# Kernel optimization log

Hardware: AMD Instinct MI355X
Metric: run time of the kernel (lower is better)

## Reference

```python
import jax, jax.numpy as jnp
import numpy as np

NEG_SLOPE = 0.2  # PyG GATConv default leaky_relu slope
EPS = 1e-16      # PyG softmax denominator epsilon


def gat_conv(x, src, dst, n_nodes, W, att_src, att_dst, bias, concat):
    # x: [N, Din]; W: [Din, H*F]; att_src/att_dst: [H, F]; bias: [H*F] or [F]
    H, F = att_src.shape
    h = (x @ W).reshape(n_nodes, H, F)                 # [N, H, F]
    a_src = jnp.einsum('nhf,hf->nh', h, att_src)       # [N, H]
    a_dst = jnp.einsum('nhf,hf->nh', h, att_dst)       # [N, H]
    e = jax.nn.leaky_relu(a_src[src] + a_dst[dst], NEG_SLOPE)  # [E, H]
    # segment softmax over incoming edges of each destination node
    m = jax.ops.segment_max(e, dst, num_segments=n_nodes)      # [N, H]
    ex = jnp.exp(e - m[dst])                                   # [E, H]
    s = jax.ops.segment_sum(ex, dst, num_segments=n_nodes)     # [N, H]
    alpha = ex / (s[dst] + EPS)                                # [E, H]
    msg = alpha[:, :, None] * h[src]                           # [E, H, F]
    out = jax.ops.segment_sum(msg, dst, num_segments=n_nodes)  # [N, H, F]
    if concat:
        out = out.reshape(n_nodes, H * F)
    else:
        out = out.mean(axis=1)
    return out + bias


def setup_inputs() -> dict:
    key = jax.random.key(0)
    ks = jax.random.split(key, 12)
    N, E, Din, Fh, H, C = 50000, 800000, 512, 32, 8, 40
    x = jax.random.normal(ks[0], (N, Din), dtype=jnp.float32)
    edge_index = jax.random.randint(ks[1], (2, E), 0, N, dtype=jnp.int64)
    g1 = 1.0 / np.sqrt(Din)
    g2 = 1.0 / np.sqrt(H * Fh)
    return {
        'x': x,
        'edge_index': edge_index,
        'W1': jax.random.normal(ks[2], (Din, H * Fh), dtype=jnp.float32) * g1,
        'att_src1': jax.random.normal(ks[3], (H, Fh), dtype=jnp.float32) * g2,
        'att_dst1': jax.random.normal(ks[4], (H, Fh), dtype=jnp.float32) * g2,
        'b1': jnp.zeros((H * Fh,), dtype=jnp.float32),
        'W2': jax.random.normal(ks[5], (H * Fh, C), dtype=jnp.float32) * g2,
        'att_src2': jax.random.normal(ks[6], (1, C), dtype=jnp.float32) * 0.1,
        'att_dst2': jax.random.normal(ks[7], (1, C), dtype=jnp.float32) * 0.1,
        'b2': jnp.zeros((C,), dtype=jnp.float32),
    }


def reference(x, edge_index, W1, att_src1, att_dst1, b1, W2, att_src2, att_dst2, b2):
    N = x.shape[0]
    # PyG GATConv adds self-loops by default
    loop = jnp.arange(N, dtype=edge_index.dtype)
    src = jnp.concatenate([edge_index[0], loop])
    dst = jnp.concatenate([edge_index[1], loop])
    # eval mode: dropout layers are identity
    h = gat_conv(x, src, dst, N, W1, att_src1, att_dst1, b1, concat=True)
    h = jax.nn.elu(h)
    out = gat_conv(h, src, dst, N, W2, att_src2, att_dst2, b2, concat=False)
    return jax.nn.log_softmax(out, axis=1)
```

## Files before the change

### kernel.cpp

```cpp
#include <hip/hip_runtime.h>
#include <hip/hip_bf16.h>
#include <math.h>

#define NN_DIN 512
#define NN_HF  256
#define NN_H   8
#define NN_F   32
#define NN_C   40

typedef short bf16x8 __attribute__((ext_vector_type(8)));
typedef float f32x4 __attribute__((ext_vector_type(4)));

__device__ __forceinline__ unsigned short f2bf_rne(float x) {
    unsigned u = __builtin_bit_cast(unsigned, x);
    unsigned r = u + 0x7FFFu + ((u >> 16) & 1u);
    return (unsigned short)(r >> 16);
}
__device__ __forceinline__ float bfu2f(unsigned short s) {
    unsigned u = ((unsigned)s) << 16;
    return __builtin_bit_cast(float, u);
}

__global__ __launch_bounds__(256) void w1rne_kernel(
    const float* __restrict__ W1, unsigned short* __restrict__ Wh)
{
    __shared__ float tile[32][33];
    int bk = blockIdx.x * 32;
    int bn = blockIdx.y * 32;
    int tx = threadIdx.x & 31, ty = threadIdx.x >> 5;
    #pragma unroll
    for (int i = 0; i < 32; i += 8)
        tile[ty + i][tx] = W1[(size_t)(bk + ty + i) * NN_HF + bn + tx];
    __syncthreads();
    #pragma unroll
    for (int i = 0; i < 32; i += 8) {
        float v = tile[tx][ty + i];
        Wh[(size_t)(bn + ty + i) * NN_DIN + bk + tx] = f2bf_rne(v);
    }
}

__global__ __launch_bounds__(256) void w2rne_kernel(
    const float* __restrict__ W2, unsigned short* __restrict__ W2T)
{
    int idx = blockIdx.x * 256 + threadIdx.x;
    if (idx >= 48 * 256) return;
    int c = idx >> 8;
    int k = idx & 255;
    unsigned short v = 0;
    if (c < NN_C) v = f2bf_rne(W2[(size_t)k * NN_C + c]);
    W2T[idx] = v;
}

#define G1_BM 64
#define G1_BN 256
#define G1_BK 64
#define G1_LDK 72

__global__ __launch_bounds__(256) void gemm1_kernel(
    const float* __restrict__ A, const unsigned short* __restrict__ BT,
    unsigned short* __restrict__ Cb, int M)
{
    __shared__ unsigned short Ah[G1_BM][G1_LDK];
    __shared__ unsigned short Bh[G1_BN][G1_LDK];
    const int m0 = blockIdx.x * G1_BM;
    const int tid = threadIdx.x;
    const int wave = tid >> 6, lane = tid & 63;
    const int wn = wave;
    const int lr = lane & 15, lg = lane >> 4;

    const int amr[4] = { (tid + 0*256) >> 4, (tid + 1*256) >> 4,
                         (tid + 2*256) >> 4, (tid + 3*256) >> 4 };
    const int akc = (tid & 15) << 2;
    const int bnr[8] = { (tid + 0*256) >> 3, (tid + 1*256) >> 3,
                         (tid + 2*256) >> 3, (tid + 3*256) >> 3,
                         (tid + 4*256) >> 3, (tid + 5*256) >> 3,
                         (tid + 6*256) >> 3, (tid + 7*256) >> 3 };
    const int bkc = (tid & 7) << 3;

    f32x4 acc[4][4];
    #pragma unroll
    for (int i = 0; i < 4; ++i)
        #pragma unroll
        for (int j = 0; j < 4; ++j) acc[i][j] = (f32x4){0.f, 0.f, 0.f, 0.f};

    float4 ra[4];
    bf16x8 rb[8];

    #pragma unroll
    for (int i = 0; i < 4; ++i) {
        ra[i] = make_float4(0.f, 0.f, 0.f, 0.f);
        if (m0 + amr[i] < M)
            ra[i] = *(const float4*)(A + (size_t)(m0 + amr[i]) * NN_DIN + akc);
    }
    #pragma unroll
    for (int i = 0; i < 8; ++i)
        rb[i] = *(const bf16x8*)(BT + (size_t)bnr[i] * NN_DIN + bkc);
    #pragma unroll
    for (int i = 0; i < 4; ++i) {
        ushort4 hv;
        hv.x = f2bf_rne(ra[i].x); hv.y = f2bf_rne(ra[i].y);
        hv.z = f2bf_rne(ra[i].z); hv.w = f2bf_rne(ra[i].w);
        *reinterpret_cast<ushort4*>(&Ah[amr[i]][akc]) = hv;
    }
    #pragma unroll
    for (int i = 0; i < 8; ++i)
        *reinterpret_cast<bf16x8*>(&Bh[bnr[i]][bkc]) = rb[i];
    __syncthreads();

    const int NSTEP = NN_DIN / G1_BK;
    for (int step = 0; step < NSTEP; ++step) {
        const bool last = (step == NSTEP - 1);
        if (!last) {
            int k0 = (step + 1) * G1_BK;
            #pragma unroll
            for (int i = 0; i < 4; ++i) {
                ra[i] = make_float4(0.f, 0.f, 0.f, 0.f);
                if (m0 + amr[i] < M)
                    ra[i] = *(const float4*)(A + (size_t)(m0 + amr[i]) * NN_DIN + k0 + akc);
            }
            #pragma unroll
            for (int i = 0; i < 8; ++i)
                rb[i] = *(const bf16x8*)(BT + (size_t)bnr[i] * NN_DIN + k0 + bkc);
        }
        #pragma unroll
        for (int ks = 0; ks < 2; ++ks) {
            const int kb = (ks << 5) + (lg << 3);
            bf16x8 fah[4], fbh[4];
            #pragma unroll
            for (int mi = 0; mi < 4; ++mi) {
                int m = (mi << 4) + lr;
                fah[mi] = *reinterpret_cast<const bf16x8*>(&Ah[m][kb]);
            }
            #pragma unroll
            for (int ni = 0; ni < 4; ++ni) {
                int n = (wn << 6) + (ni << 4) + lr;
                fbh[ni] = *reinterpret_cast<const bf16x8*>(&Bh[n][kb]);
            }
            #pragma unroll
            for (int mi = 0; mi < 4; ++mi)
                #pragma unroll
                for (int ni = 0; ni < 4; ++ni)
                    acc[mi][ni] = __builtin_amdgcn_mfma_f32_16x16x32_bf16(
                        fah[mi], fbh[ni], acc[mi][ni], 0, 0, 0);
        }
        __syncthreads();
        if (!last) {
            #pragma unroll
            for (int i = 0; i < 4; ++i) {
                ushort4 hv;
                hv.x = f2bf_rne(ra[i].x); hv.y = f2bf_rne(ra[i].y);
                hv.z = f2bf_rne(ra[i].z); hv.w = f2bf_rne(ra[i].w);
                *reinterpret_cast<ushort4*>(&Ah[amr[i]][akc]) = hv;
            }
            #pragma unroll
            for (int i = 0; i < 8; ++i)
                *reinterpret_cast<bf16x8*>(&Bh[bnr[i]][bkc]) = rb[i];
            __syncthreads();
        }
    }
    #pragma unroll
    for (int mi = 0; mi < 4; ++mi)
        #pragma unroll
        for (int ni = 0; ni < 4; ++ni)
            #pragma unroll
            for (int r = 0; r < 4; ++r) {
                int row = m0 + (mi << 4) + (lg << 2) + r;
                int col = (wn << 6) + (ni << 4) + lr;
                if (row < M)
                    Cb[(size_t)row * NN_HF + col] = f2bf_rne(acc[mi][ni][r]);
            }
}

__global__ __launch_bounds__(256) void attn1_kernel(
    const unsigned short* __restrict__ h1b, const float* __restrict__ att_s,
    const float* __restrict__ att_d, float* __restrict__ a1s,
    float* __restrict__ a1d)
{
    int n = blockIdx.x;
    int t = threadIdx.x;
    float hv = bfu2f(h1b[(size_t)n * NN_HF + t]);
    float ps = hv * att_s[t];
    float pd = hv * att_d[t];
    #pragma unroll
    for (int off = 16; off >= 1; off >>= 1) {
        ps += __shfl_down(ps, off, 32);
        pd += __shfl_down(pd, off, 32);
    }
    if ((t & 31) == 0) {
        a1s[n * NN_H + (t >> 5)] = ps;
        a1d[n * NN_H + (t >> 5)] = pd;
    }
}

__global__ void count_kernel(const int* __restrict__ dst, int* __restrict__ deg,
                             int E, int Nn)
{
    int e = blockIdx.x * blockDim.x + threadIdx.x;
    int Et = E + Nn;
    if (e >= Et) return;
    int d = (e < E) ? dst[e] : (e - E);
    atomicAdd(&deg[d], 1);
}

#define SCAN_CHUNK 1024
__global__ __launch_bounds__(256) void scan1_kernel(
    const int* __restrict__ deg, int* __restrict__ offs,
    int* __restrict__ bsums, int Nn)
{
    __shared__ int sh[256];
    int b = blockIdx.x, t = threadIdx.x;
    int base = b * SCAN_CHUNK + t * 4;
    int v[4];
    int tot = 0;
    #pragma unroll
    for (int i = 0; i < 4; ++i) {
        v[i] = (base + i < Nn) ? deg[base + i] : 0;
        tot += v[i];
    }
    sh[t] = tot;
    __syncthreads();
    for (int off = 1; off < 256; off <<= 1) {
        int y = (t >= off) ? sh[t - off] : 0;
        __syncthreads();
        sh[t] += y;
        __syncthreads();
    }
    int p = sh[t] - tot;
    #pragma unroll
    for (int i = 0; i < 4; ++i) {
        if (base + i < Nn) offs[base + i] = p;
        p += v[i];
    }
    if (t == 255) bsums[b] = sh[255];
}

__global__ void scan2_kernel(int* __restrict__ bsums, int nb)
{
    if (threadIdx.x == 0) {
        int run = 0;
        for (int i = 0; i < nb; ++i) {
            int tmp = bsums[i];
            bsums[i] = run;
            run += tmp;
        }
    }
}

__global__ void scan3_kernel(int* __restrict__ offs, const int* __restrict__ bsums,
                             int Nn, int Et)
{
    int i = blockIdx.x * blockDim.x + threadIdx.x;
    if (i < Nn) offs[i] += bsums[i >> 10];
    if (i == 0) offs[Nn] = Et;
}

__global__ void fill_kernel(const int* __restrict__ src, const int* __restrict__ dst,
                            const int* __restrict__ offs, int* __restrict__ cursor,
                            int* __restrict__ srcs, int E, int Nn)
{
    int e = blockIdx.x * blockDim.x + threadIdx.x;
    int Et = E + Nn;
    if (e >= Et) return;
    int d, s;
    if (e < E) { d = dst[e]; s = src[e]; }
    else       { d = e - E;  s = e - E;  }
    int pos = offs[d] + atomicAdd(&cursor[d], 1);
    srcs[pos] = s;
}

__global__ __launch_bounds__(256) void agg1_kernel(
    const unsigned short* __restrict__ h1b, const float* __restrict__ a1s,
    const float* __restrict__ a1d, const int* __restrict__ offs,
    const int* __restrict__ srcs, const float* __restrict__ b1,
    unsigned short* __restrict__ hp1b, int Nn)
{
    int n = blockIdx.x * 4 + (threadIdx.x >> 6);
    if (n >= Nn) return;
    int lane = threadIdx.x & 63;
    int beg = offs[n], end = offs[n + 1];

    int g = lane >> 3, hh = lane & 7;
    float adn1 = a1d[n * NN_H + hh];
    float m = -3.0e38f, s = 0.f;
    for (int k = beg + g; k < end; k += 8) {
        float e = a1s[srcs[k] * NN_H + hh] + adn1;
        e = e > 0.f ? e : 0.2f * e;
        float nm = fmaxf(m, e);
        s = s * __expf(m - nm) + __expf(e - nm);
        m = nm;
    }
    #pragma unroll
    for (int off = 8; off < 64; off <<= 1) {
        float mo = __shfl_xor(m, off);
        float so = __shfl_xor(s, off);
        float nm = fmaxf(m, mo);
        s = s * __expf(m - nm) + so * __expf(mo - nm);
        m = nm;
    }
    float inv = 1.f / (s + 1e-16f);

    int h = lane >> 3;
    float mh   = __shfl(m, h);
    float invh = __shfl(inv, h);
    float adn  = __shfl(adn1, h);

    f32x4 a0 = {0.f,0.f,0.f,0.f}, a1 = a0, a2 = a0, a3 = a0;
    int k = beg;
    for (; k + 3 < end; k += 4) {
        int s0 = srcs[k], s1 = srcs[k+1], s2 = srcs[k+2], s3 = srcs[k+3];
        float e0 = a1s[s0 * NN_H + h] + adn;
        float e1 = a1s[s1 * NN_H + h] + adn;
        float e2 = a1s[s2 * NN_H + h] + adn;
        float e3 = a1s[s3 * NN_H + h] + adn;
        e0 = e0 > 0.f ? e0 : 0.2f * e0;  e1 = e1 > 0.f ? e1 : 0.2f * e1;
        e2 = e2 > 0.f ? e2 : 0.2f * e2;  e3 = e3 > 0.f ? e3 : 0.2f * e3;
        float w0 = __expf(e0 - mh) * invh;
        float w1 = __expf(e1 - mh) * invh;
        float w2 = __expf(e2 - mh) * invh;
        float w3 = __expf(e3 - mh) * invh;
        ushort4 v0 = *(const ushort4*)(h1b + (size_t)s0 * NN_HF + lane * 4);
        ushort4 v1 = *(const ushort4*)(h1b + (size_t)s1 * NN_HF + lane * 4);
        ushort4 v2 = *(const ushort4*)(h1b + (size_t)s2 * NN_HF + lane * 4);
        ushort4 v3 = *(const ushort4*)(h1b + (size_t)s3 * NN_HF + lane * 4);
        a0.x = fmaf(w0, bfu2f(v0.x), a0.x); a0.y = fmaf(w0, bfu2f(v0.y), a0.y);
        a0.z = fmaf(w0, bfu2f(v0.z), a0.z); a0.w = fmaf(w0, bfu2f(v0.w), a0.w);
        a1.x = fmaf(w1, bfu2f(v1.x), a1.x); a1.y = fmaf(w1, bfu2f(v1.y), a1.y);
        a1.z = fmaf(w1, bfu2f(v1.z), a1.z); a1.w = fmaf(w1, bfu2f(v1.w), a1.w);
        a2.x = fmaf(w2, bfu2f(v2.x), a2.x); a2.y = fmaf(w2, bfu2f(v2.y), a2.y);
        a2.z = fmaf(w2, bfu2f(v2.z), a2.z); a2.w = fmaf(w2, bfu2f(v2.w), a2.w);
        a3.x = fmaf(w3, bfu2f(v3.x), a3.x); a3.y = fmaf(w3, bfu2f(v3.y), a3.y);
        a3.z = fmaf(w3, bfu2f(v3.z), a3.z); a3.w = fmaf(w3, bfu2f(v3.w), a3.w);
    }
    for (; k < end; ++k) {
        int s0 = srcs[k];
        float e0 = a1s[s0 * NN_H + h] + adn;
        e0 = e0 > 0.f ? e0 : 0.2f * e0;
        float w0 = __expf(e0 - mh) * invh;
        ushort4 v0 = *(const ushort4*)(h1b + (size_t)s0 * NN_HF + lane * 4);
        a0.x = fmaf(w0, bfu2f(v0.x), a0.x); a0.y = fmaf(w0, bfu2f(v0.y), a0.y);
        a0.z = fmaf(w0, bfu2f(v0.z), a0.z); a0.w = fmaf(w0, bfu2f(v0.w), a0.w);
    }
    f32x4 acc;
    acc[0] = (a0.x + a1.x) + (a2.x + a3.x);
    acc[1] = (a0.y + a1.y) + (a2.y + a3.y);
    acc[2] = (a0.z + a1.z) + (a2.z + a3.z);
    acc[3] = (a0.w + a1.w) + (a2.w + a3.w);
    float4 bb = *(const float4*)(b1 + lane * 4);
    float r0 = acc[0] + bb.x, r1 = acc[1] + bb.y;
    float r2 = acc[2] + bb.z, r3 = acc[3] + bb.w;
    r0 = r0 > 0.f ? r0 : __expf(r0) - 1.f;
    r1 = r1 > 0.f ? r1 : __expf(r1) - 1.f;
    r2 = r2 > 0.f ? r2 : __expf(r2) - 1.f;
    r3 = r3 > 0.f ? r3 : __expf(r3) - 1.f;
    ushort4 o = make_ushort4(f2bf_rne(r0), f2bf_rne(r1), f2bf_rne(r2), f2bf_rne(r3));
    *(ushort4*)(hp1b + (size_t)n * NN_HF + lane * 4) = o;
}

#define G2_BM 128

__global__ __launch_bounds__(256) void gemm2_kernel(
    const unsigned short* __restrict__ Ab, const unsigned short* __restrict__ W2T,
    const float* __restrict__ att_s, const float* __restrict__ att_d,
    float* __restrict__ h2, float* __restrict__ a2s, float* __restrict__ a2d,
    int M)
{
    __shared__ unsigned short Ah[G2_BM][72];
    __shared__ unsigned short Bh[48][72];
    const int m0 = blockIdx.x * G2_BM;
    const int tid = threadIdx.x;
    const int wave = tid >> 6, lane = tid & 63;
    const int lr = lane & 15, lg = lane >> 4;

    f32x4 acc[2][3];
    #pragma unroll
    for (int i = 0; i < 2; ++i)
        #pragma unroll
        for (int j = 0; j < 3; ++j) acc[i][j] = (f32x4){0.f, 0.f, 0.f, 0.f};

    for (int kc = 0; kc < NN_HF; kc += 64) {
        #pragma unroll
        for (int i = 0; i < 4; ++i) {
            int gi = tid + i * 256;
            int r = gi >> 3;
            int k8 = (gi & 7) << 3;
            bf16x8 v = (bf16x8){0,0,0,0,0,0,0,0};
            if (m0 + r < M)
                v = *(const bf16x8*)(Ab + (size_t)(m0 + r) * NN_HF + kc + k8);
            *reinterpret_cast<bf16x8*>(&Ah[r][k8]) = v;
        }
        #pragma unroll
        for (int i = 0; i < 2; ++i) {
            int gi = tid + i * 256;
            if (gi < 384) {
                int r = gi >> 3;
                int k8 = (gi & 7) << 3;
                *reinterpret_cast<bf16x8*>(&Bh[r][k8]) =
                    *(const bf16x8*)(W2T + (size_t)r * NN_HF + kc + k8);
            }
        }
        __syncthreads();
        #pragma unroll
        for (int ks = 0; ks < 2; ++ks) {
            const int kb = (ks << 5) + (lg << 3);
            bf16x8 fa[2], fb[3];
            #pragma unroll
            for (int mi = 0; mi < 2; ++mi) {
                int r = (wave << 5) + (mi << 4) + lr;
                fa[mi] = *reinterpret_cast<const bf16x8*>(&Ah[r][kb]);
            }
            #pragma unroll
            for (int ni = 0; ni < 3; ++ni) {
                int c = (ni << 4) + lr;
                fb[ni] = *reinterpret_cast<const bf16x8*>(&Bh[c][kb]);
            }
            #pragma unroll
            for (int mi = 0; mi < 2; ++mi)
                #pragma unroll
                for (int ni = 0; ni < 3; ++ni)
                    acc[mi][ni] = __builtin_amdgcn_mfma_f32_16x16x32_bf16(
                        fa[mi], fb[ni], acc[mi][ni], 0, 0, 0);
        }
        __syncthreads();
    }

    float asv[3], adv[3];
    #pragma unroll
    for (int ni = 0; ni < 3; ++ni) {
        int c = (ni << 4) + lr;
        asv[ni] = (c < NN_C) ? att_s[c] : 0.f;
        adv[ni] = (c < NN_C) ? att_d[c] : 0.f;
    }
    #pragma unroll
    for (int mi = 0; mi < 2; ++mi) {
        float ps[4] = {0.f,0.f,0.f,0.f}, pd[4] = {0.f,0.f,0.f,0.f};
        #pragma unroll
        for (int ni = 0; ni < 3; ++ni) {
            int c = (ni << 4) + lr;
            #pragma unroll
            for (int r = 0; r < 4; ++r) {
                float v = acc[mi][ni][r];
                ps[r] = fmaf(v, asv[ni], ps[r]);
                pd[r] = fmaf(v, adv[ni], pd[r]);
                int row = m0 + (wave << 5) + (mi << 4) + (lg << 2) + r;
                if (c < NN_C && row < M)
                    h2[(size_t)row * NN_C + c] = v;
            }
        }
        #pragma unroll
        for (int off = 1; off < 16; off <<= 1) {
            #pragma unroll
            for (int r = 0; r < 4; ++r) {
                ps[r] += __shfl_xor(ps[r], off);
                pd[r] += __shfl_xor(pd[r], off);
            }
        }
        if (lr == 0) {
            #pragma unroll
            for (int r = 0; r < 4; ++r) {
                int row = m0 + (wave << 5) + (mi << 4) + (lg << 2) + r;
                if (row < M) { a2s[row] = ps[r]; a2d[row] = pd[r]; }
            }
        }
    }
}

__global__ __launch_bounds__(256) void agg2_kernel(
    const float* __restrict__ h2, const float* __restrict__ a2s,
    const float* __restrict__ a2d, const int* __restrict__ offs,
    const int* __restrict__ srcs, const float* __restrict__ b2,
    float* __restrict__ out, int Nn)
{
    int n = blockIdx.x * 4 + (threadIdx.x >> 6);
    if (n >= Nn) return;
    int f = threadIdx.x & 63;
    int beg = offs[n], end = offs[n + 1];
    float adn = a2d[n];

    float m = -3.0e38f, s = 0.f;
    for (int k = beg + f; k < end; k += 64) {
        float e = a2s[srcs[k]] + adn;
        e = e > 0.f ? e : 0.2f * e;
        float nm = fmaxf(m, e);
        s = s * __expf(m - nm) + __expf(e - nm);
        m = nm;
    }
    #pragma unroll
    for (int off = 1; off < 64; off <<= 1) {
        float mo = __shfl_xor(m, off);
        float so = __shfl_xor(s, off);
        float nm = fmaxf(m, mo);
        s = s * __expf(m - nm) + so * __expf(mo - nm);
        m = nm;
    }
    float inv = 1.f / (s + 1e-16f);

    float a0 = 0.f, a1 = 0.f, a2 = 0.f, a3 = 0.f;
    int k = beg;
    for (; k + 3 < end; k += 4) {
        int s0 = srcs[k], s1 = srcs[k+1], s2 = srcs[k+2], s3 = srcs[k+3];
        float e0 = a2s[s0] + adn, e1 = a2s[s1] + adn;
        float e2 = a2s[s2] + adn, e3 = a2s[s3] + adn;
        e0 = e0 > 0.f ? e0 : 0.2f * e0;  e1 = e1 > 0.f ? e1 : 0.2f * e1;
        e2 = e2 > 0.f ? e2 : 0.2f * e2;  e3 = e3 > 0.f ? e3 : 0.2f * e3;
        float w0 = __expf(e0 - m) * inv, w1 = __expf(e1 - m) * inv;
        float w2 = __expf(e2 - m) * inv, w3 = __expf(e3 - m) * inv;
        float h0 = (f < NN_C) ? h2[(size_t)s0 * NN_C + f] : 0.f;
        float h1 = (f < NN_C) ? h2[(size_t)s1 * NN_C + f] : 0.f;
        float h2v = (f < NN_C) ? h2[(size_t)s2 * NN_C + f] : 0.f;
        float h3 = (f < NN_C) ? h2[(size_t)s3 * NN_C + f] : 0.f;
        a0 = fmaf(w0, h0, a0); a1 = fmaf(w1, h1, a1);
        a2 = fmaf(w2, h2v, a2); a3 = fmaf(w3, h3, a3);
    }
    for (; k < end; ++k) {
        int s0 = srcs[k];
        float e0 = a2s[s0] + adn;
        e0 = e0 > 0.f ? e0 : 0.2f * e0;
        float w0 = __expf(e0 - m) * inv;
        float h0 = (f < NN_C) ? h2[(size_t)s0 * NN_C + f] : 0.f;
        a0 = fmaf(w0, h0, a0);
    }
    float acc = (a0 + a1) + (a2 + a3);
    float v = acc + ((f < NN_C) ? b2[f] : 0.f);
    float lg = (f < NN_C) ? v : -INFINITY;
    float mx = lg;
    #pragma unroll
    for (int off = 32; off >= 1; off >>= 1) mx = fmaxf(mx, __shfl_xor(mx, off));
    float w2e = (f < NN_C) ? __expf(lg - mx) : 0.f;
    float sum = w2e;
    #pragma unroll
    for (int off = 32; off >= 1; off >>= 1) sum += __shfl_xor(sum, off);
    if (f < NN_C) out[(size_t)n * NN_C + f] = lg - mx - __logf(sum);
}

extern "C" void kernel_launch(void* const* d_in, const int* in_sizes, int n_in,
                              void* d_out, int out_size, void* d_ws, size_t ws_size,
                              hipStream_t stream)
{
    const float* x    = (const float*)d_in[0];
    const int*   ei   = (const int*)d_in[1];
    const float* W1   = (const float*)d_in[2];
    const float* as1  = (const float*)d_in[3];
    const float* ad1  = (const float*)d_in[4];
    const float* b1   = (const float*)d_in[5];
    const float* W2   = (const float*)d_in[6];
    const float* as2  = (const float*)d_in[7];
    const float* ad2  = (const float*)d_in[8];
    const float* b2   = (const float*)d_in[9];
    float* out = (float*)d_out;

    int Nn = in_sizes[0] / NN_DIN;
    int E  = in_sizes[1] / 2;
    int Et = E + Nn;
    const int* srcIdx = ei;
    const int* dstIdx = ei + E;

    char* ws = (char*)d_ws;
    size_t off = 0;
    auto alloc = [&](size_t bytes) {
        void* p = ws + off;
        off = (off + bytes + 255) & ~(size_t)255;
        return p;
    };
    unsigned short* h1b  = (unsigned short*)alloc((size_t)Nn * NN_HF * 2);
    unsigned short* W1T  = (unsigned short*)alloc((size_t)NN_HF * NN_DIN * 2);
    unsigned short* W2T  = (unsigned short*)alloc((size_t)48 * NN_HF * 2);
    unsigned short* hp1b = (unsigned short*)alloc((size_t)Nn * NN_HF * 2);
    float* a1s  = (float*)alloc((size_t)Nn * NN_H * 4);
    float* a1d  = (float*)alloc((size_t)Nn * NN_H * 4);
    float* h2   = (float*)alloc((size_t)Nn * NN_C * 4);
    float* a2s  = (float*)alloc((size_t)Nn * 4);
    float* a2d  = (float*)alloc((size_t)Nn * 4);
    int*   deg  = (int*)alloc((size_t)Nn * 4);
    int*   offs = (int*)alloc((size_t)(Nn + 1) * 4);
    int*   bsums= (int*)alloc(1024 * 4);
    int*   curs = (int*)alloc((size_t)Nn * 4);
    int*   srcs = (int*)alloc((size_t)Et * 4);

    hipMemsetAsync(deg, 0, (size_t)Nn * 4, stream);
    hipMemsetAsync(curs, 0, (size_t)Nn * 4, stream);

    w1rne_kernel<<<dim3(NN_DIN / 32, NN_HF / 32), 256, 0, stream>>>(W1, W1T);
    w2rne_kernel<<<48, 256, 0, stream>>>(W2, W2T);

    gemm1_kernel<<<(Nn + G1_BM - 1) / G1_BM, 256, 0, stream>>>(x, W1T, h1b, Nn);

    attn1_kernel<<<Nn, 256, 0, stream>>>(h1b, as1, ad1, a1s, a1d);

    count_kernel<<<(Et + 255) / 256, 256, 0, stream>>>(dstIdx, deg, E, Nn);
    int nb = (Nn + SCAN_CHUNK - 1) / SCAN_CHUNK;
    scan1_kernel<<<nb, 256, 0, stream>>>(deg, offs, bsums, Nn);
    scan2_kernel<<<1, 64, 0, stream>>>(bsums, nb);
    scan3_kernel<<<(Nn + 255) / 256, 256, 0, stream>>>(offs, bsums, Nn, Et);
    fill_kernel<<<(Et + 255) / 256, 256, 0, stream>>>(srcIdx, dstIdx, offs, curs, srcs, E, Nn);

    agg1_kernel<<<(Nn + 3) / 4, 256, 0, stream>>>(h1b, a1s, a1d, offs, srcs, b1, hp1b, Nn);

    gemm2_kernel<<<(Nn + G2_BM - 1) / G2_BM, 256, 0, stream>>>(
        hp1b, W2T, as2, ad2, h2, a2s, a2d, Nn);

    agg2_kernel<<<(Nn + 3) / 4, 256, 0, stream>>>(h2, a2s, a2d, offs, srcs, b2, out, Nn);
}
```

Measured before the change: 440.2 us.

## Fuse attention logits into GEMM1, drop softmax max pass, widen agg1 loads

```diff
diff --git a/kernel.cpp b/kernel.cpp
--- a/kernel.cpp
+++ b/kernel.cpp
@@ -58,7 +58,9 @@
 
 __global__ __launch_bounds__(256) void gemm1_kernel(
     const float* __restrict__ A, const unsigned short* __restrict__ BT,
-    unsigned short* __restrict__ Cb, int M)
+    const float* __restrict__ as1, const float* __restrict__ ad1,
+    unsigned short* __restrict__ Cb, float* __restrict__ a1s,
+    float* __restrict__ a1d, int M)
 {
     __shared__ unsigned short Ah[G1_BM][G1_LDK];
     __shared__ unsigned short Bh[G1_BN][G1_LDK];
@@ -158,38 +160,41 @@
             __syncthreads();
         }
     }
+    float asv[4], adv[4];
+    #pragma unroll
+    for (int ni = 0; ni < 4; ++ni) {
+        int c = (wn << 6) + (ni << 4) + lr;
+        asv[ni] = as1[c]; adv[ni] = ad1[c];
+    }
     #pragma unroll
     for (int mi = 0; mi < 4; ++mi)
         #pragma unroll
-        for (int ni = 0; ni < 4; ++ni)
-            #pragma unroll
-            for (int r = 0; r < 4; ++r) {
-                int row = m0 + (mi << 4) + (lg << 2) + r;
-                int col = (wn << 6) + (ni << 4) + lr;
-                if (row < M)
-                    Cb[(size_t)row * NN_HF + col] = f2bf_rne(acc[mi][ni][r]);
-            }
-}
-
-__global__ __launch_bounds__(256) void attn1_kernel(
-    const unsigned short* __restrict__ h1b, const float* __restrict__ att_s,
-    const float* __restrict__ att_d, float* __restrict__ a1s,
-    float* __restrict__ a1d)
-{
-    int n = blockIdx.x;
-    int t = threadIdx.x;
-    float hv = bfu2f(h1b[(size_t)n * NN_HF + t]);
-    float ps = hv * att_s[t];
-    float pd = hv * att_d[t];
-    #pragma unroll
-    for (int off = 16; off >= 1; off >>= 1) {
-        ps += __shfl_down(ps, off, 32);
-        pd += __shfl_down(pd, off, 32);
-    }
-    if ((t & 31) == 0) {
-        a1s[n * NN_H + (t >> 5)] = ps;
-        a1d[n * NN_H + (t >> 5)] = pd;
-    }
+        for (int r = 0; r < 4; ++r) {
+            int row = m0 + (mi << 4) + (lg << 2) + r;
+            float v0 = acc[mi][0][r], v1 = acc[mi][1][r];
+            float v2 = acc[mi][2][r], v3 = acc[mi][3][r];
+            if (row < M) {
+                Cb[(size_t)row * NN_HF + (wn << 6) + (0 << 4) + lr] = f2bf_rne(v0);
+                Cb[(size_t)row * NN_HF + (wn << 6) + (1 << 4) + lr] = f2bf_rne(v1);
+                Cb[(size_t)row * NN_HF + (wn << 6) + (2 << 4) + lr] = f2bf_rne(v2);
+                Cb[(size_t)row * NN_HF + (wn << 6) + (3 << 4) + lr] = f2bf_rne(v3);
+            }
+            float ps0 = v0 * asv[0] + v1 * asv[1];
+            float pd0 = v0 * adv[0] + v1 * adv[1];
+            float ps1 = v2 * asv[2] + v3 * asv[3];
+            float pd1 = v2 * adv[2] + v3 * adv[3];
+            #pragma unroll
+            for (int off = 1; off < 16; off <<= 1) {
+                ps0 += __shfl_xor(ps0, off); pd0 += __shfl_xor(pd0, off);
+                ps1 += __shfl_xor(ps1, off); pd1 += __shfl_xor(pd1, off);
+            }
+            if (lr == 0 && row < M) {
+                a1s[row * NN_H + 2 * wn]     = ps0;
+                a1s[row * NN_H + 2 * wn + 1] = ps1;
+                a1d[row * NN_H + 2 * wn]     = pd0;
+                a1d[row * NN_H + 2 * wn + 1] = pd1;
+            }
+        }
 }
 
 __global__ void count_kernel(const int* __restrict__ dst, int* __restrict__ deg,
@@ -281,79 +286,83 @@
 
     int g = lane >> 3, hh = lane & 7;
     float adn1 = a1d[n * NN_H + hh];
-    float m = -3.0e38f, s = 0.f;
+    float s = 0.f;
     for (int k = beg + g; k < end; k += 8) {
         float e = a1s[srcs[k] * NN_H + hh] + adn1;
         e = e > 0.f ? e : 0.2f * e;
-        float nm = fmaxf(m, e);
-        s = s * __expf(m - nm) + __expf(e - nm);
-        m = nm;
-    }
-    #pragma unroll
-    for (int off = 8; off < 64; off <<= 1) {
-        float mo = __shfl_xor(m, off);
-        float so = __shfl_xor(s, off);
-        float nm = fmaxf(m, mo);
-        s = s * __expf(m - nm) + so * __expf(mo - nm);
-        m = nm;
-    }
+        s += __expf(e);
+    }
+    #pragma unroll
+    for (int off = 8; off < 64; off <<= 1) s += __shfl_xor(s, off);
     float inv = 1.f / (s + 1e-16f);
 
-    int h = lane >> 3;
-    float mh   = __shfl(m, h);
+    int hl = lane & 31;
+    int h = hl >> 2;
+    int half = lane >> 5;
     float invh = __shfl(inv, h);
     float adn  = __shfl(adn1, h);
 
-    f32x4 a0 = {0.f,0.f,0.f,0.f}, a1 = a0, a2 = a0, a3 = a0;
+    float c0[8] = {0,0,0,0,0,0,0,0};
+    float c1[8] = {0,0,0,0,0,0,0,0};
     int k = beg;
     for (; k + 3 < end; k += 4) {
-        int s0 = srcs[k], s1 = srcs[k+1], s2 = srcs[k+2], s3 = srcs[k+3];
+        int s0 = srcs[k + half];
+        int s1 = srcs[k + 2 + half];
         float e0 = a1s[s0 * NN_H + h] + adn;
         float e1 = a1s[s1 * NN_H + h] + adn;
-        float e2 = a1s[s2 * NN_H + h] + adn;
-        float e3 = a1s[s3 * NN_H + h] + adn;
-        e0 = e0 > 0.f ? e0 : 0.2f * e0;  e1 = e1 > 0.f ? e1 : 0.2f * e1;
-        e2 = e2 > 0.f ? e2 : 0.2f * e2;  e3 = e3 > 0.f ? e3 : 0.2f * e3;
-        float w0 = __expf(e0 - mh) * invh;
-        float w1 = __expf(e1 - mh) * invh;
-        float w2 = __expf(e2 - mh) * invh;
-        float w3 = __expf(e3 - mh) * invh;
-        ushort4 v0 = *(const ushort4*)(h1b + (size_t)s0 * NN_HF + lane * 4);
-        ushort4 v1 = *(const ushort4*)(h1b + (size_t)s1 * NN_HF + lane * 4);
-        ushort4 v2 = *(const ushort4*)(h1b + (size_t)s2 * NN_HF + lane * 4);
-        ushort4 v3 = *(const ushort4*)(h1b + (size_t)s3 * NN_HF + lane * 4);
-        a0.x = fmaf(w0, bfu2f(v0.x), a0.x); a0.y = fmaf(w0, bfu2f(v0.y), a0.y);
-        a0.z = fmaf(w0, bfu2f(v0.z), a0.z); a0.w = fmaf(w0, bfu2f(v0.w), a0.w);
-        a1.x = fmaf(w1, bfu2f(v1.x), a1.x); a1.y = fmaf(w1, bfu2f(v1.y), a1.y);
-        a1.z = fmaf(w1, bfu2f(v1.z), a1.z); a1.w = fmaf(w1, bfu2f(v1.w), a1.w);
-        a2.x = fmaf(w2, bfu2f(v2.x), a2.x); a2.y = fmaf(w2, bfu2f(v2.y), a2.y);
-        a2.z = fmaf(w2, bfu2f(v2.z), a2.z); a2.w = fmaf(w2, bfu2f(v2.w), a2.w);
-        a3.x = fmaf(w3, bfu2f(v3.x), a3.x); a3.y = fmaf(w3, bfu2f(v3.y), a3.y);
-        a3.z = fmaf(w3, bfu2f(v3.z), a3.z); a3.w = fmaf(w3, bfu2f(v3.w), a3.w);
-    }
-    for (; k < end; ++k) {
+        e0 = e0 > 0.f ? e0 : 0.2f * e0;
+        e1 = e1 > 0.f ? e1 : 0.2f * e1;
+        float w0 = __expf(e0) * invh;
+        float w1 = __expf(e1) * invh;
+        bf16x8 v0 = *(const bf16x8*)(h1b + (size_t)s0 * NN_HF + hl * 8);
+        bf16x8 v1 = *(const bf16x8*)(h1b + (size_t)s1 * NN_HF + hl * 8);
+        #pragma unroll
+        for (int j = 0; j < 8; ++j) {
+            c0[j] = fmaf(w0, bfu2f((unsigned short)v0[j]), c0[j]);
+            c1[j] = fmaf(w1, bfu2f((unsigned short)v1[j]), c1[j]);
+        }
+    }
+    for (; k + 1 < end; k += 2) {
+        int s0 = srcs[k + half];
+        float e0 = a1s[s0 * NN_H + h] + adn;
+        e0 = e0 > 0.f ? e0 : 0.2f * e0;
+        float w0 = __expf(e0) * invh;
+        bf16x8 v0 = *(const bf16x8*)(h1b + (size_t)s0 * NN_HF + hl * 8);
+        #pragma unroll
+        for (int j = 0; j < 8; ++j)
+            c0[j] = fmaf(w0, bfu2f((unsigned short)v0[j]), c0[j]);
+    }
+    if (k < end) {
         int s0 = srcs[k];
         float e0 = a1s[s0 * NN_H + h] + adn;
         e0 = e0 > 0.f ? e0 : 0.2f * e0;
-        float w0 = __expf(e0 - mh) * invh;
-        ushort4 v0 = *(const ushort4*)(h1b + (size_t)s0 * NN_HF + lane * 4);
-        a0.x = fmaf(w0, bfu2f(v0.x), a0.x); a0.y = fmaf(w0, bfu2f(v0.y), a0.y);
-        a0.z = fmaf(w0, bfu2f(v0.z), a0.z); a0.w = fmaf(w0, bfu2f(v0.w), a0.w);
-    }
-    f32x4 acc;
-    acc[0] = (a0.x + a1.x) + (a2.x + a3.x);
-    acc[1] = (a0.y + a1.y) + (a2.y + a3.y);
-    acc[2] = (a0.z + a1.z) + (a2.z + a3.z);
-    acc[3] = (a0.w + a1.w) + (a2.w + a3.w);
-    float4 bb = *(const float4*)(b1 + lane * 4);
-    float r0 = acc[0] + bb.x, r1 = acc[1] + bb.y;
-    float r2 = acc[2] + bb.z, r3 = acc[3] + bb.w;
-    r0 = r0 > 0.f ? r0 : __expf(r0) - 1.f;
-    r1 = r1 > 0.f ? r1 : __expf(r1) - 1.f;
-    r2 = r2 > 0.f ? r2 : __expf(r2) - 1.f;
-    r3 = r3 > 0.f ? r3 : __expf(r3) - 1.f;
-    ushort4 o = make_ushort4(f2bf_rne(r0), f2bf_rne(r1), f2bf_rne(r2), f2bf_rne(r3));
-    *(ushort4*)(hp1b + (size_t)n * NN_HF + lane * 4) = o;
+        float w0 = (half == 0) ? __expf(e0) * invh : 0.f;
+        bf16x8 v0 = *(const bf16x8*)(h1b + (size_t)s0 * NN_HF + hl * 8);
+        #pragma unroll
+        for (int j = 0; j < 8; ++j)
+            c0[j] = fmaf(w0, bfu2f((unsigned short)v0[j]), c0[j]);
+    }
+    #pragma unroll
+    for (int j = 0; j < 8; ++j) {
+        c0[j] += c1[j];
+        c0[j] += __shfl_xor(c0[j], 32);
+    }
+    if (half == 0) {
+        float4 bb0 = *(const float4*)(b1 + hl * 8);
+        float4 bb1 = *(const float4*)(b1 + hl * 8 + 4);
+        float r[8];
+        r[0] = c0[0] + bb0.x; r[1] = c0[1] + bb0.y;
+        r[2] = c0[2] + bb0.z; r[3] = c0[3] + bb0.w;
+        r[4] = c0[4] + bb1.x; r[5] = c0[5] + bb1.y;
+        r[6] = c0[6] + bb1.z; r[7] = c0[7] + bb1.w;
+        bf16x8 ov;
+        #pragma unroll
+        for (int j = 0; j < 8; ++j) {
+            float v = r[j] > 0.f ? r[j] : __expf(r[j]) - 1.f;
+            ov[j] = (short)f2bf_rne(v);
+        }
+        *(bf16x8*)(hp1b + (size_t)n * NN_HF + hl * 8) = ov;
+    }
 }
 
 #define G2_BM 128
@@ -476,22 +485,14 @@
     int beg = offs[n], end = offs[n + 1];
     float adn = a2d[n];
 
-    float m = -3.0e38f, s = 0.f;
+    float s = 0.f;
     for (int k = beg + f; k < end; k += 64) {
         float e = a2s[srcs[k]] + adn;
         e = e > 0.f ? e : 0.2f * e;
-        float nm = fmaxf(m, e);
-        s = s * __expf(m - nm) + __expf(e - nm);
-        m = nm;
-    }
-    #pragma unroll
-    for (int off = 1; off < 64; off <<= 1) {
-        float mo = __shfl_xor(m, off);
-        float so = __shfl_xor(s, off);
-        float nm = fmaxf(m, mo);
-        s = s * __expf(m - nm) + so * __expf(mo - nm);
-        m = nm;
-    }
+        s += __expf(e);
+    }
+    #pragma unroll
+    for (int off = 1; off < 64; off <<= 1) s += __shfl_xor(s, off);
     float inv = 1.f / (s + 1e-16f);
 
     float a0 = 0.f, a1 = 0.f, a2 = 0.f, a3 = 0.f;
@@ -502,8 +503,8 @@
         float e2 = a2s[s2] + adn, e3 = a2s[s3] + adn;
         e0 = e0 > 0.f ? e0 : 0.2f * e0;  e1 = e1 > 0.f ? e1 : 0.2f * e1;
         e2 = e2 > 0.f ? e2 : 0.2f * e2;  e3 = e3 > 0.f ? e3 : 0.2f * e3;
-        float w0 = __expf(e0 - m) * inv, w1 = __expf(e1 - m) * inv;
-        float w2 = __expf(e2 - m) * inv, w3 = __expf(e3 - m) * inv;
+        float w0 = __expf(e0) * inv, w1 = __expf(e1) * inv;
+        float w2 = __expf(e2) * inv, w3 = __expf(e3) * inv;
         float h0 = (f < NN_C) ? h2[(size_t)s0 * NN_C + f] : 0.f;
         float h1 = (f < NN_C) ? h2[(size_t)s1 * NN_C + f] : 0.f;
         float h2v = (f < NN_C) ? h2[(size_t)s2 * NN_C + f] : 0.f;
@@ -515,7 +516,7 @@
         int s0 = srcs[k];
         float e0 = a2s[s0] + adn;
         e0 = e0 > 0.f ? e0 : 0.2f * e0;
-        float w0 = __expf(e0 - m) * inv;
+        float w0 = __expf(e0) * inv;
         float h0 = (f < NN_C) ? h2[(size_t)s0 * NN_C + f] : 0.f;
         a0 = fmaf(w0, h0, a0);
     }
@@ -582,9 +583,8 @@
     w1rne_kernel<<<dim3(NN_DIN / 32, NN_HF / 32), 256, 0, stream>>>(W1, W1T);
     w2rne_kernel<<<48, 256, 0, stream>>>(W2, W2T);
 
-    gemm1_kernel<<<(Nn + G1_BM - 1) / G1_BM, 256, 0, stream>>>(x, W1T, h1b, Nn);
-
-    attn1_kernel<<<Nn, 256, 0, stream>>>(h1b, as1, ad1, a1s, a1d);
+    gemm1_kernel<<<(Nn + G1_BM - 1) / G1_BM, 256, 0, stream>>>(
+        x, W1T, as1, ad1, h1b, a1s, a1d, Nn);
 
     count_kernel<<<(Et + 255) / 256, 256, 0, stream>>>(dstIdx, deg, E, Nn);
     int nb = (Nn + SCAN_CHUNK - 1) / SCAN_CHUNK;
```

New measurement: 420.5 us. 1.05x faster.
